# Kernel optimization log

Hardware: AMD Instinct MI355X
Metric: run time of the kernel (lower is better)

## Reference

```python
import jax, jax.numpy as jnp
import numpy as np

B, T, E, H, V = 64, 21, 512, 512, 10000


def _lstm_step(x, h, c, W_ih, W_hh, b):
    # PyTorch LSTMCell gate order: i, f, g, o
    gates = x @ W_ih.T + h @ W_hh.T + b  # [B, 4H]
    i, f, g, o = jnp.split(gates, 4, axis=-1)
    i, f, o = jax.nn.sigmoid(i), jax.nn.sigmoid(f), jax.nn.sigmoid(o)
    g = jnp.tanh(g)
    c_new = f * c + i * g
    h_new = o * jnp.tanh(c_new)
    return h_new, c_new


def setup_inputs() -> dict:
    key = jax.random.key(0)
    ks = jax.random.split(key, 8)
    s_ih = 1.0 / np.sqrt(H)
    return {
        "features": jax.random.normal(ks[0], (B, E), jnp.float32),
        "caption_embedding": jax.random.normal(ks[1], (B, T, E), jnp.float32),
        "W_ih": jax.random.uniform(ks[2], (4 * H, E), jnp.float32, -s_ih, s_ih),
        "W_hh": jax.random.uniform(ks[3], (4 * H, H), jnp.float32, -s_ih, s_ih),
        "b_ih": jax.random.uniform(ks[4], (4 * H,), jnp.float32, -s_ih, s_ih),
        "b_hh": jax.random.uniform(ks[5], (4 * H,), jnp.float32, -s_ih, s_ih),
        "W_lin": jax.random.uniform(ks[6], (V, H), jnp.float32, -s_ih, s_ih),
        "b_lin": jax.random.uniform(ks[7], (V,), jnp.float32, -s_ih, s_ih),
    }


def reference(features, caption_embedding, W_ih, W_hh, b_ih, b_hh, W_lin, b_lin):
    b = b_ih + b_hh
    batch = features.shape[0]
    hidden = W_hh.shape[1]
    h0 = jnp.zeros((batch, hidden), features.dtype)
    c0 = jnp.zeros((batch, hidden), features.dtype)
    # t = 0: consume image features, no output emitted
    h, c = _lstm_step(features, h0, c0, W_ih, W_hh, b)
    # t = 1..T-1: consume caption_embedding[:, t-1], emit linear(h)
    emb_seq = jnp.swapaxes(caption_embedding[:, :-1, :], 0, 1)  # [T-1, B, E]

    def body(carry, x_t):
        h, c = carry
        h, c = _lstm_step(x_t, h, c, W_ih, W_hh, b)
        out = h @ W_lin.T + b_lin  # [B, V]
        return (h, c), out

    _, outs = jax.lax.scan(body, (h, c), emb_seq)  # [T-1, B, V]
    return jnp.swapaxes(outs, 0, 1)  # [B, T-1, V]
```

## Files before the change

kernel.cpp:

```cpp
#include <hip/hip_runtime.h>
#include <hip/hip_bf16.h>


#define NB 64
#define NT 21
#define NE 512
#define NH 512
#define NV 10000
#define G4 2048
#define FLGD 16

typedef __attribute__((ext_vector_type(8))) short bf16x8;
typedef __attribute__((ext_vector_type(4))) float f32x4;
typedef __attribute__((ext_vector_type(4))) unsigned short u16x4;

#define OFF_WIH_HI   0UL
#define OFF_WIH_LO   2097152UL
#define OFF_WHH_HI   4194304UL
#define OFF_WHH_LO   6291456UL
#define OFF_WLIN_HI  8388608UL
#define OFF_XSEQ_HI  18743296UL
#define OFF_XSEQ_LO  20185088UL
#define OFF_BIAS     21626880UL
#define OFF_XIH      21635072UL
#define OFF_GHH      32645120UL
#define OFF_GHL      32776192UL
#define OFF_C        32907264UL
#define OFF_HBUF     33038336UL
#define OFF_FLG      34349056UL

__device__ inline unsigned short f2bf(float f) {
    unsigned int u = __float_as_uint(f);
    unsigned int r = u + 0x7FFFu + ((u >> 16) & 1u);
    return (unsigned short)(r >> 16);
}
__device__ inline float bf2f(unsigned short s) {
    return __uint_as_float(((unsigned int)s) << 16);
}

__device__ __forceinline__ void gl_lds16(const unsigned short* g, unsigned short* l) {
    auto gp = (const __attribute__((address_space(1))) unsigned int*)(unsigned long long)(const void*)g;
    auto lp = (__attribute__((address_space(3))) unsigned int*)(unsigned int)(unsigned long long)(void*)l;
    __builtin_amdgcn_global_load_lds(gp, lp, 16, 0, 0);
}

__device__ __forceinline__ void gl_lds16_sc(const unsigned short* g, unsigned short* l) {
    auto gp = (const __attribute__((address_space(1))) unsigned int*)(unsigned long long)(const void*)g;
    auto lp = (__attribute__((address_space(3))) unsigned int*)(unsigned int)(unsigned long long)(void*)l;
    __builtin_amdgcn_global_load_lds(gp, lp, 16, 0, 17);
}

__device__ __forceinline__ void st4_sc(unsigned int* p, unsigned int v) {
    asm volatile("global_store_dword %0, %1, off sc0 sc1" :: "v"(p), "v"(v) : "memory");
}

__global__ __launch_bounds__(256) void prep_kernel(
    const float* __restrict__ features, const float* __restrict__ cap,
    const float* __restrict__ W_ih, const float* __restrict__ b_ih,
    const float* __restrict__ b_hh, const float* __restrict__ W_lin,
    unsigned char* __restrict__ ws)
{
    const int idx = blockIdx.x * 256 + threadIdx.x;
    unsigned short* wih_hi = (unsigned short*)(ws + OFF_WIH_HI);
    unsigned short* wih_lo = (unsigned short*)(ws + OFF_WIH_LO);
    unsigned short* wlin_hi = (unsigned short*)(ws + OFF_WLIN_HI);
    unsigned short* xs_hi = (unsigned short*)(ws + OFF_XSEQ_HI);
    unsigned short* xs_lo = (unsigned short*)(ws + OFF_XSEQ_LO);
    float* bias = (float*)(ws + OFF_BIAS);

    if (idx < 262144) {
        const int i4 = idx * 4;
        float4 w = *(const float4*)(W_ih + i4);
        u16x4 hi, lo;
        hi.x = f2bf(w.x); lo.x = f2bf(w.x - bf2f(hi.x));
        hi.y = f2bf(w.y); lo.y = f2bf(w.y - bf2f(hi.y));
        hi.z = f2bf(w.z); lo.z = f2bf(w.z - bf2f(hi.z));
        hi.w = f2bf(w.w); lo.w = f2bf(w.w - bf2f(hi.w));
        *(u16x4*)(wih_hi + i4) = hi;
        *(u16x4*)(wih_lo + i4) = lo;
    } else if (idx < 1542144) {
        const int i4 = (idx - 262144) * 4;
        float4 w = *(const float4*)(W_lin + i4);
        u16x4 hi;
        hi.x = f2bf(w.x); hi.y = f2bf(w.y); hi.z = f2bf(w.z); hi.w = f2bf(w.w);
        *(u16x4*)(wlin_hi + i4) = hi;
    } else if (idx < 1714176) {
        const int i4 = (idx - 1542144) * 4;
        const int e = i4 & 511;
        const int b = (i4 >> 9) & 63;
        const int t = i4 >> 15;
        float4 x = (t == 0) ? *(const float4*)(features + b * NE + e)
                            : *(const float4*)(cap + b * (NT * NE) + (t - 1) * NE + e);
        u16x4 hi, lo;
        hi.x = f2bf(x.x); lo.x = f2bf(x.x - bf2f(hi.x));
        hi.y = f2bf(x.y); lo.y = f2bf(x.y - bf2f(hi.y));
        hi.z = f2bf(x.z); lo.z = f2bf(x.z - bf2f(hi.z));
        hi.w = f2bf(x.w); lo.w = f2bf(x.w - bf2f(hi.w));
        *(u16x4*)(xs_hi + i4) = hi;
        *(u16x4*)(xs_lo + i4) = lo;
    } else if (idx < 1714688) {
        const int j = (idx - 1714176) * 4;
        float4 a = *(const float4*)(b_ih + j);
        float4 b = *(const float4*)(b_hh + j);
        *(float4*)(bias + j) = make_float4(a.x + b.x, a.y + b.y, a.z + b.z, a.w + b.w);
    }
}

__global__ __launch_bounds__(512) void fused_persistent(
    unsigned char* __restrict__ ws, const float* __restrict__ W_hh_f,
    const float* __restrict__ b_lin, float* __restrict__ out)
{
    __shared__ unsigned short Hhi[64 * 512];
    __shared__ unsigned short Hlo[64 * 512];
    __shared__ float glf[4096];
    const int tid = threadIdx.x;
    const int lane = tid & 63, wv = tid >> 6;
    const int mf = lane & 15, kg = lane >> 4;

    unsigned int* __restrict__ flg = (unsigned int*)(ws + OFF_C);
    unsigned int* __restrict__ slabctr = (unsigned int*)(ws + OFF_FLG);
    unsigned short* __restrict__ hbuf = (unsigned short*)(ws + OFF_HBUF);
    const unsigned short* __restrict__ wlin = (const unsigned short*)(ws + OFF_WLIN_HI);
    const float* __restrict__ bias = (const float*)(ws + OFF_BIAS);
    float* __restrict__ xih_base = (float*)(ws + OFF_XIH);

    if (blockIdx.x < 32) {
        const int bc = blockIdx.x;
        const int q = wv & 3;
        const int mh = wv >> 2;

        unsigned short* __restrict__ ghh = (unsigned short*)(ws + OFF_GHH);
        unsigned short* __restrict__ ghl = (unsigned short*)(ws + OFF_GHL);

        bf16x8 bh[16], blo[16];
#pragma unroll
        for (int j = 0; j < 16; ++j) {
            const float* src = W_hh_f + (size_t)(q * 512 + bc * 16 + mf) * 512 + j * 32 + kg * 8;
            float4 w0 = *(const float4*)src;
            float4 w1 = *(const float4*)(src + 4);
            float ff[8] = {w0.x, w0.y, w0.z, w0.w, w1.x, w1.y, w1.z, w1.w};
#pragma unroll
            for (int e = 0; e < 8; ++e) {
                const unsigned short h = f2bf(ff[e]);
                bh[j][e] = (short)h;
                blo[j][e] = (short)f2bf(ff[e] - bf2f(h));
            }
        }

        const int crow = tid >> 3;
        const int cp = tid & 7;
        const int c0 = bc * 16 + cp * 2;
        const int jc0 = c0 >> 3;
        float creg0 = 0.f, creg1 = 0.f;

        float2 xp[4];
        auto load_xp = [&](int tt) {
            const float* __restrict__ xq = xih_base + (size_t)tt * NB * G4;
#pragma unroll
            for (int g2 = 0; g2 < 4; ++g2)
                xp[g2] = *(const float2*)&xq[crow * G4 + g2 * 512 + c0];
        };

        if (tid == 0) {
            while (__hip_atomic_load(&slabctr[0], __ATOMIC_RELAXED, __HIP_MEMORY_SCOPE_AGENT) < 16u)
                __builtin_amdgcn_s_sleep(1);
        }
        __syncthreads();
        load_xp(0);

        for (int t = 0; t < NT; ++t) {
            f32x4 acc[2];
            acc[0] = (f32x4){0.f, 0.f, 0.f, 0.f};
            acc[1] = (f32x4){0.f, 0.f, 0.f, 0.f};

            if (t > 0) {
                const int rd = (t + 1) & 1;
                const unsigned short* __restrict__ ghh_r = ghh + rd * (NB * NH);
                const unsigned short* __restrict__ ghl_r = ghl + rd * (NB * NH);
#pragma unroll
                for (int i = 0; i < 8; ++i) {
                    const int s = i * 512 + tid;
                    gl_lds16_sc(ghh_r + s * 8, &Hhi[s * 8]);
                }
#pragma unroll
                for (int i = 0; i < 8; ++i) {
                    const int s = i * 512 + tid;
                    gl_lds16_sc(ghl_r + s * 8, &Hlo[s * 8]);
                }
                asm volatile("s_waitcnt vmcnt(8)" ::: "memory");
                __builtin_amdgcn_s_barrier();
#pragma unroll
                for (int kt = 0; kt < 16; ++kt) {
                    const int j = kt * 4 + kg;
#pragma unroll
                    for (int m = 0; m < 2; ++m) {
                        const int row = mh * 32 + m * 16 + mf;
                        bf16x8 a_hi = *(const bf16x8*)&Hhi[(row * 64 + (j ^ (row & 7))) * 8];
                        acc[m] = __builtin_amdgcn_mfma_f32_16x16x32_bf16(a_hi, bh[kt], acc[m], 0, 0, 0);
                        acc[m] = __builtin_amdgcn_mfma_f32_16x16x32_bf16(a_hi, blo[kt], acc[m], 0, 0, 0);
                    }
                }
                asm volatile("s_waitcnt vmcnt(0)" ::: "memory");
                __builtin_amdgcn_s_barrier();
#pragma unroll
                for (int kt = 0; kt < 16; ++kt) {
                    const int j = kt * 4 + kg;
#pragma unroll
                    for (int m = 0; m < 2; ++m) {
                        const int row = mh * 32 + m * 16 + mf;
                        bf16x8 a_lo = *(const bf16x8*)&Hlo[(row * 64 + (j ^ (row & 7))) * 8];
                        acc[m] = __builtin_amdgcn_mfma_f32_16x16x32_bf16(a_lo, bh[kt], acc[m], 0, 0, 0);
                    }
                }
            }

#pragma unroll
            for (int m = 0; m < 2; ++m) {
                const int row = mh * 32 + m * 16 + kg * 4;
#pragma unroll
                for (int r = 0; r < 4; ++r)
                    glf[(q * 64 + row + r) * 16 + mf] = acc[m][r];
            }
            __syncthreads();

            {
                unsigned short* __restrict__ ghh_w = ghh + (t & 1) * (NB * NH);
                unsigned short* __restrict__ ghl_w = ghl + (t & 1) * (NB * NH);
                const float2 g0 = *(const float2*)&glf[(0 * 64 + crow) * 16 + cp * 2];
                const float2 g1 = *(const float2*)&glf[(1 * 64 + crow) * 16 + cp * 2];
                const float2 g2 = *(const float2*)&glf[(2 * 64 + crow) * 16 + cp * 2];
                const float2 g3 = *(const float2*)&glf[(3 * 64 + crow) * 16 + cp * 2];
                const float gi0 = g0.x + xp[0].x, gi1 = g0.y + xp[0].y;
                const float gf0 = g1.x + xp[1].x, gf1 = g1.y + xp[1].y;
                const float gg0 = g2.x + xp[2].x, gg1 = g2.y + xp[2].y;
                const float go0 = g3.x + xp[3].x, go1 = g3.y + xp[3].y;
                const float i0 = 1.f / (1.f + __expf(-gi0)), i1 = 1.f / (1.f + __expf(-gi1));
                const float f0 = 1.f / (1.f + __expf(-gf0)), f1 = 1.f / (1.f + __expf(-gf1));
                const float ga0 = tanhf(gg0),                ga1 = tanhf(gg1);
                const float o0 = 1.f / (1.f + __expf(-go0)), o1 = 1.f / (1.f + __expf(-go1));
                const float cn0 = f0 * creg0 + i0 * ga0;
                const float cn1 = f1 * creg1 + i1 * ga1;
                creg0 = cn0; creg1 = cn1;
                const float h0 = o0 * tanhf(cn0);
                const float h1 = o1 * tanhf(cn1);
                const unsigned short hi0 = f2bf(h0), hi1 = f2bf(h1);
                const unsigned short lo0 = f2bf(h0 - bf2f(hi0)), lo1 = f2bf(h1 - bf2f(hi1));
                const unsigned int hpack = (unsigned int)hi0 | ((unsigned int)hi1 << 16);
                const unsigned int lpack = (unsigned int)lo0 | ((unsigned int)lo1 << 16);
                const int sw = crow * 512 + ((jc0 ^ (crow & 7)) << 3) + (cp & 3) * 2;
                st4_sc((unsigned int*)&ghh_w[sw], hpack);
                st4_sc((unsigned int*)&ghl_w[sw], lpack);
                if (t >= 1)
                    st4_sc((unsigned int*)&hbuf[(size_t)(t - 1) * (NB * NH) + crow * NH + c0], hpack);
            }

            asm volatile("s_waitcnt vmcnt(0)" ::: "memory");
            __syncthreads();
            if (tid == 0) {
                unsigned int one = 1u;
                unsigned int* fp = flg + ((size_t)t * 32 + bc) * FLGD;
                asm volatile("global_store_dword %0, %1, off sc0 sc1" :: "v"(fp), "v"(one) : "memory");
            }
            if (t < NT - 1) {
                if (tid == 0) {
                    while (__hip_atomic_load(&slabctr[(t + 1) * FLGD], __ATOMIC_RELAXED, __HIP_MEMORY_SCOPE_AGENT) < 16u)
                        __builtin_amdgcn_s_sleep(1);
                }
                __syncthreads();
                load_xp(t + 1);
                if (wv == 0) {
                    const unsigned int* fp = flg + ((size_t)t * 32 + (lane & 31)) * FLGD;
                    while (__hip_atomic_load(fp, __ATOMIC_RELAXED, __HIP_MEMORY_SCOPE_AGENT) == 0u)
                        __builtin_amdgcn_s_sleep(1);
                }
                __syncthreads();
            }
        }
        asm volatile("s_waitcnt vmcnt(0)" ::: "memory");
        return;
    }

    const int g = blockIdx.x - 32;
    const int mw2 = (wv >> 2) * 32, nw2 = (wv & 3) * 32;

    {
        const unsigned short* __restrict__ xh = (const unsigned short*)(ws + OFF_XSEQ_HI);
        const unsigned short* __restrict__ xl = (const unsigned short*)(ws + OFF_XSEQ_LO);
        const unsigned short* __restrict__ wih_h = (const unsigned short*)(ws + OFF_WIH_HI);
        const unsigned short* __restrict__ wih_l = (const unsigned short*)(ws + OFF_WIH_LO);

        unsigned short* Ah2 = Hhi;
        unsigned short* Al2 = Hhi + 4096;
        unsigned short* Bh2 = Hhi + 8192;
        unsigned short* Bl2 = Hhi + 16384;

        const int ntile = (g < 112) ? 2 : 1;
        for (int p = 0; p < ntile; ++p) {
            const int T = (p == 0) ? g : 224 + g;
            const int slab = T >> 4, ct = T & 15;
            const unsigned short* __restrict__ xhA = xh + (size_t)slab * 64 * 512;
            const unsigned short* __restrict__ xlA = xl + (size_t)slab * 64 * 512;

            auto stageA = [&](int buf, int k0) {
                if (tid < 256) {
                    const int s = tid, r = s >> 2, kc = (s & 3) * 8;
                    gl_lds16(xhA + (size_t)r * 512 + k0 + kc, &Ah2[buf * 2048 + s * 8]);
                    gl_lds16(xlA + (size_t)r * 512 + k0 + kc, &Al2[buf * 2048 + s * 8]);
                } else {
#pragma unroll
                    for (int h2 = 0; h2 < 2; ++h2) {
                        const int s = h2 * 256 + (tid - 256), r = s >> 2, kc = (s & 3) * 8;
                        gl_lds16(wih_h + (size_t)(ct * 128 + r) * 512 + k0 + kc, &Bh2[buf * 4096 + s * 8]);
                        gl_lds16(wih_l + (size_t)(ct * 128 + r) * 512 + k0 + kc, &Bl2[buf * 4096 + s * 8]);
                    }
                }
            };

            f32x4 acc2[2][2];
#pragma unroll
            for (int i = 0; i < 2; i++)
#pragma unroll
                for (int j = 0; j < 2; j++) acc2[i][j] = (f32x4){0.f, 0.f, 0.f, 0.f};

            stageA(0, 0);
            for (int kt = 0; kt < 16; ++kt) {
                __syncthreads();
                const int cur = kt & 1;
                if (kt < 15) stageA(cur ^ 1, (kt + 1) * 32);
                bf16x8 ah_[2], al_[2], bh_[2], bl_[2];
#pragma unroll
                for (int i = 0; i < 2; i++) {
                    ah_[i] = *(const bf16x8*)&Ah2[cur * 2048 + (mw2 + i * 16 + mf) * 32 + kg * 8];
                    al_[i] = *(const bf16x8*)&Al2[cur * 2048 + (mw2 + i * 16 + mf) * 32 + kg * 8];
                    bh_[i] = *(const bf16x8*)&Bh2[cur * 4096 + (nw2 + i * 16 + mf) * 32 + kg * 8];
                    bl_[i] = *(const bf16x8*)&Bl2[cur * 4096 + (nw2 + i * 16 + mf) * 32 + kg * 8];
                }
#pragma unroll
                for (int i = 0; i < 2; i++)
#pragma unroll
                    for (int j = 0; j < 2; j++) {
                        acc2[i][j] = __builtin_amdgcn_mfma_f32_16x16x32_bf16(ah_[i], bh_[j], acc2[i][j], 0, 0, 0);
                        acc2[i][j] = __builtin_amdgcn_mfma_f32_16x16x32_bf16(ah_[i], bl_[j], acc2[i][j], 0, 0, 0);
                        acc2[i][j] = __builtin_amdgcn_mfma_f32_16x16x32_bf16(al_[i], bh_[j], acc2[i][j], 0, 0, 0);
                    }
            }
#pragma unroll
            for (int i = 0; i < 2; i++)
#pragma unroll
                for (int j = 0; j < 2; j++) {
                    const int col = ct * 128 + nw2 + j * 16 + mf;
                    const float bb = bias[col];
#pragma unroll
                    for (int r = 0; r < 4; r++) {
                        const int row = slab * 64 + mw2 + i * 16 + kg * 4 + r;
                        st4_sc((unsigned int*)&xih_base[(size_t)row * G4 + col],
                               __float_as_uint(acc2[i][j][r] + bb));
                    }
                }
            asm volatile("s_waitcnt vmcnt(0)" ::: "memory");
            __syncthreads();
            if (tid == 0)
                __hip_atomic_fetch_add(&slabctr[slab * FLGD], 1u, __ATOMIC_RELAXED, __HIP_MEMORY_SCOPE_AGENT);
            __syncthreads();
        }
    }

    const int jt = g % 79;
    const int rshare = g / 79;
    const int nshare = (jt < 66) ? 3 : 2;
    const int n0g = jt * 128;

    unsigned short* __restrict__ AsB = Hhi;
    unsigned short* __restrict__ BsB = Hhi + 4096;

    for (int tt = rshare; tt < NT - 1; tt += nshare) {
        if (wv == 0) {
            const unsigned int* fp = flg + ((size_t)(tt + 1) * 32 + (lane & 31)) * FLGD;
            while (__hip_atomic_load(fp, __ATOMIC_RELAXED, __HIP_MEMORY_SCOPE_AGENT) == 0u)
                __builtin_amdgcn_s_sleep(2);
        }
        __syncthreads();

        const unsigned short* __restrict__ hbA = hbuf + (size_t)tt * (NB * NH);
        auto stageC = [&](int buf, int k0) {
            if (tid < 256) {
                const int s = tid;
                const int r = s >> 2, kcol = (s & 3) * 8;
                gl_lds16_sc(hbA + (size_t)r * 512 + k0 + kcol, &AsB[buf * 2048 + s * 8]);
            } else {
#pragma unroll
                for (int h2 = 0; h2 < 2; ++h2) {
                    const int s = h2 * 256 + (tid - 256);
                    const int r = s >> 2, kcol = (s & 3) * 8;
                    gl_lds16(wlin + (size_t)(n0g + r) * 512 + k0 + kcol, &BsB[buf * 4096 + s * 8]);
                }
            }
        };

        f32x4 acc2[2][2];
#pragma unroll
        for (int i = 0; i < 2; i++)
#pragma unroll
            for (int j = 0; j < 2; j++) acc2[i][j] = (f32x4){0.f, 0.f, 0.f, 0.f};

        stageC(0, 0);
        for (int kt = 0; kt < 16; ++kt) {
            __syncthreads();
            const int cur = kt & 1;
            if (kt < 15) stageC(cur ^ 1, (kt + 1) * 32);
            bf16x8 af[2], bfv[2];
#pragma unroll
            for (int i = 0; i < 2; i++) {
                af[i]  = *(const bf16x8*)&AsB[cur * 2048 + (mw2 + i * 16 + mf) * 32 + kg * 8];
                bfv[i] = *(const bf16x8*)&BsB[cur * 4096 + (nw2 + i * 16 + mf) * 32 + kg * 8];
            }
#pragma unroll
            for (int i = 0; i < 2; i++)
#pragma unroll
                for (int j = 0; j < 2; j++)
                    acc2[i][j] = __builtin_amdgcn_mfma_f32_16x16x32_bf16(af[i], bfv[j], acc2[i][j], 0, 0, 0);
        }
#pragma unroll
        for (int i = 0; i < 2; i++)
#pragma unroll
            for (int j = 0; j < 2; j++) {
                const int col = n0g + nw2 + j * 16 + mf;
                if (col < NV) {
                    const float bl = b_lin[col];
#pragma unroll
                    for (int r = 0; r < 4; r++) {
                        const int b_ = mw2 + i * 16 + kg * 4 + r;
                        out[(size_t)b_ * ((NT - 1) * NV) + (size_t)tt * NV + col] = acc2[i][j][r] + bl;
                    }
                }
            }
        __syncthreads();
    }
}

extern "C" void kernel_launch(void* const* d_in, const int* in_sizes, int n_in,
                              void* d_out, int out_size, void* d_ws, size_t ws_size,
                              hipStream_t stream)
{
    const float* features = (const float*)d_in[0];
    const float* cap      = (const float*)d_in[1];
    const float* W_ih     = (const float*)d_in[2];
    const float* W_hh     = (const float*)d_in[3];
    const float* b_ih     = (const float*)d_in[4];
    const float* b_hh     = (const float*)d_in[5];
    const float* W_lin    = (const float*)d_in[6];
    const float* b_lin    = (const float*)d_in[7];
    float* out = (float*)d_out;
    unsigned char* ws = (unsigned char*)d_ws;

    hipMemsetAsync(ws + OFF_C, 0, (size_t)NT * 32 * FLGD * sizeof(unsigned int), stream);
    hipMemsetAsync(ws + OFF_FLG, 0, (size_t)NT * FLGD * sizeof(unsigned int), stream);

    hipLaunchKernelGGL(prep_kernel, dim3(6698), dim3(256), 0, stream,
                       features, cap, W_ih, b_ih, b_hh, W_lin, ws);
    hipLaunchKernelGGL(fused_persistent, dim3(256), dim3(512), 0, stream, ws, W_hh, b_lin, out);
}
```

Baseline: 251.0 us.

## Fuse prep conversion into persistent kernel and defer W_lin conversion behind recurrence

Removes the separate prep kernel launch and moves the fp32-to-bf16 split of W_ih, inputs and bias into the start of the persistent kernel, guarded by a grid-wide counter. The W_lin bf16 conversion is now done by the 224 non-recurrent blocks after their input-projection GEMM, so it overlaps with the LSTM recurrence, followed by a barrier among those blocks. The recurrent blocks also merge their two waits (slab counter and step flags) into a single wait. The risk is extra spin barriers on all blocks being co-resident, and the start of the recurrence is now delayed until every block finishes prep.

```diff
diff --git a/kernel.cpp b/kernel.cpp
--- a/kernel.cpp
+++ b/kernel.cpp
@@ -53,62 +53,19 @@
 __device__ __forceinline__ void st4_sc(unsigned int* p, unsigned int v) {
     asm volatile("global_store_dword %0, %1, off sc0 sc1" :: "v"(p), "v"(v) : "memory");
 }
-
-__global__ __launch_bounds__(256) void prep_kernel(
+__device__ __forceinline__ void st8_sc(unsigned short* p, u16x4 v) {
+    asm volatile("global_store_dwordx2 %0, %1, off sc0 sc1" :: "v"(p), "v"(v) : "memory");
+}
+__device__ __forceinline__ void st16_sc(float* p, f32x4 v) {
+    asm volatile("global_store_dwordx4 %0, %1, off sc0 sc1" :: "v"(p), "v"(v) : "memory");
+}
+
+__global__ __launch_bounds__(512) void fused_all(
     const float* __restrict__ features, const float* __restrict__ cap,
-    const float* __restrict__ W_ih, const float* __restrict__ b_ih,
-    const float* __restrict__ b_hh, const float* __restrict__ W_lin,
-    unsigned char* __restrict__ ws)
-{
-    const int idx = blockIdx.x * 256 + threadIdx.x;
-    unsigned short* wih_hi = (unsigned short*)(ws + OFF_WIH_HI);
-    unsigned short* wih_lo = (unsigned short*)(ws + OFF_WIH_LO);
-    unsigned short* wlin_hi = (unsigned short*)(ws + OFF_WLIN_HI);
-    unsigned short* xs_hi = (unsigned short*)(ws + OFF_XSEQ_HI);
-    unsigned short* xs_lo = (unsigned short*)(ws + OFF_XSEQ_LO);
-    float* bias = (float*)(ws + OFF_BIAS);
-
-    if (idx < 262144) {
-        const int i4 = idx * 4;
-        float4 w = *(const float4*)(W_ih + i4);
-        u16x4 hi, lo;
-        hi.x = f2bf(w.x); lo.x = f2bf(w.x - bf2f(hi.x));
-        hi.y = f2bf(w.y); lo.y = f2bf(w.y - bf2f(hi.y));
-        hi.z = f2bf(w.z); lo.z = f2bf(w.z - bf2f(hi.z));
-        hi.w = f2bf(w.w); lo.w = f2bf(w.w - bf2f(hi.w));
-        *(u16x4*)(wih_hi + i4) = hi;
-        *(u16x4*)(wih_lo + i4) = lo;
-    } else if (idx < 1542144) {
-        const int i4 = (idx - 262144) * 4;
-        float4 w = *(const float4*)(W_lin + i4);
-        u16x4 hi;
-        hi.x = f2bf(w.x); hi.y = f2bf(w.y); hi.z = f2bf(w.z); hi.w = f2bf(w.w);
-        *(u16x4*)(wlin_hi + i4) = hi;
-    } else if (idx < 1714176) {
-        const int i4 = (idx - 1542144) * 4;
-        const int e = i4 & 511;
-        const int b = (i4 >> 9) & 63;
-        const int t = i4 >> 15;
-        float4 x = (t == 0) ? *(const float4*)(features + b * NE + e)
-                            : *(const float4*)(cap + b * (NT * NE) + (t - 1) * NE + e);
-        u16x4 hi, lo;
-        hi.x = f2bf(x.x); lo.x = f2bf(x.x - bf2f(hi.x));
-        hi.y = f2bf(x.y); lo.y = f2bf(x.y - bf2f(hi.y));
-        hi.z = f2bf(x.z); lo.z = f2bf(x.z - bf2f(hi.z));
-        hi.w = f2bf(x.w); lo.w = f2bf(x.w - bf2f(hi.w));
-        *(u16x4*)(xs_hi + i4) = hi;
-        *(u16x4*)(xs_lo + i4) = lo;
-    } else if (idx < 1714688) {
-        const int j = (idx - 1714176) * 4;
-        float4 a = *(const float4*)(b_ih + j);
-        float4 b = *(const float4*)(b_hh + j);
-        *(float4*)(bias + j) = make_float4(a.x + b.x, a.y + b.y, a.z + b.z, a.w + b.w);
-    }
-}
-
-__global__ __launch_bounds__(512) void fused_persistent(
-    unsigned char* __restrict__ ws, const float* __restrict__ W_hh_f,
-    const float* __restrict__ b_lin, float* __restrict__ out)
+    const float* __restrict__ W_ih_f, const float* __restrict__ W_hh_f,
+    const float* __restrict__ b_ih, const float* __restrict__ b_hh,
+    const float* __restrict__ W_lin_f, const float* __restrict__ b_lin,
+    float* __restrict__ out, unsigned char* __restrict__ ws)
 {
     __shared__ unsigned short Hhi[64 * 512];
     __shared__ unsigned short Hlo[64 * 512];
@@ -120,9 +77,55 @@
     unsigned int* __restrict__ flg = (unsigned int*)(ws + OFF_C);
     unsigned int* __restrict__ slabctr = (unsigned int*)(ws + OFF_FLG);
     unsigned short* __restrict__ hbuf = (unsigned short*)(ws + OFF_HBUF);
-    const unsigned short* __restrict__ wlin = (const unsigned short*)(ws + OFF_WLIN_HI);
     const float* __restrict__ bias = (const float*)(ws + OFF_BIAS);
     float* __restrict__ xih_base = (float*)(ws + OFF_XIH);
+
+    {
+        unsigned short* wih_hi = (unsigned short*)(ws + OFF_WIH_HI);
+        unsigned short* wih_lo = (unsigned short*)(ws + OFF_WIH_LO);
+        unsigned short* xs_hi = (unsigned short*)(ws + OFF_XSEQ_HI);
+        unsigned short* xs_lo = (unsigned short*)(ws + OFF_XSEQ_LO);
+        float* bias_w = (float*)(ws + OFF_BIAS);
+        int idx = blockIdx.x * 512 + tid;
+        for (int it = 0; it < 4; ++it, idx += 131072) {
+            if (idx < 262144) {
+                const int i4 = idx * 4;
+                float4 w = *(const float4*)(W_ih_f + i4);
+                u16x4 hi, lo;
+                hi.x = f2bf(w.x); lo.x = f2bf(w.x - bf2f(hi.x));
+                hi.y = f2bf(w.y); lo.y = f2bf(w.y - bf2f(hi.y));
+                hi.z = f2bf(w.z); lo.z = f2bf(w.z - bf2f(hi.z));
+                hi.w = f2bf(w.w); lo.w = f2bf(w.w - bf2f(hi.w));
+                st8_sc(wih_hi + i4, hi);
+                st8_sc(wih_lo + i4, lo);
+            } else if (idx < 434176) {
+                const int i4 = (idx - 262144) * 4;
+                const int e = i4 & 511;
+                const int b = (i4 >> 9) & 63;
+                const int t2 = i4 >> 15;
+                float4 x = (t2 == 0) ? *(const float4*)(features + b * NE + e)
+                                     : *(const float4*)(cap + b * (NT * NE) + (t2 - 1) * NE + e);
+                u16x4 hi, lo;
+                hi.x = f2bf(x.x); lo.x = f2bf(x.x - bf2f(hi.x));
+                hi.y = f2bf(x.y); lo.y = f2bf(x.y - bf2f(hi.y));
+                hi.z = f2bf(x.z); lo.z = f2bf(x.z - bf2f(hi.z));
+                hi.w = f2bf(x.w); lo.w = f2bf(x.w - bf2f(hi.w));
+                st8_sc(xs_hi + i4, hi);
+                st8_sc(xs_lo + i4, lo);
+            } else if (idx < 434688) {
+                const int j = (idx - 434176) * 4;
+                float4 a = *(const float4*)(b_ih + j);
+                float4 b = *(const float4*)(b_hh + j);
+                f32x4 s;
+                s[0] = a.x + b.x; s[1] = a.y + b.y; s[2] = a.z + b.z; s[3] = a.w + b.w;
+                st16_sc(bias_w + j, s);
+            }
+        }
+        asm volatile("s_waitcnt vmcnt(0)" ::: "memory");
+        __syncthreads();
+        if (tid == 0)
+            __hip_atomic_fetch_add(&slabctr[24 * FLGD], 1u, __ATOMIC_RELAXED, __HIP_MEMORY_SCOPE_AGENT);
+    }
 
     if (blockIdx.x < 32) {
         const int bc = blockIdx.x;
@@ -262,18 +265,19 @@
                 asm volatile("global_store_dword %0, %1, off sc0 sc1" :: "v"(fp), "v"(one) : "memory");
             }
             if (t < NT - 1) {
-                if (tid == 0) {
-                    while (__hip_atomic_load(&slabctr[(t + 1) * FLGD], __ATOMIC_RELAXED, __HIP_MEMORY_SCOPE_AGENT) < 16u)
-                        __builtin_amdgcn_s_sleep(1);
+                if (wv == 0) {
+                    if (lane < 32) {
+                        const unsigned int* fp = flg + ((size_t)t * 32 + lane) * FLGD;
+                        while (__hip_atomic_load(fp, __ATOMIC_RELAXED, __HIP_MEMORY_SCOPE_AGENT) == 0u)
+                            __builtin_amdgcn_s_sleep(1);
+                    } else if (lane == 32) {
+                        const unsigned int* sp = slabctr + (size_t)(t + 1) * FLGD;
+                        while (__hip_atomic_load(sp, __ATOMIC_RELAXED, __HIP_MEMORY_SCOPE_AGENT) < 16u)
+                            __builtin_amdgcn_s_sleep(1);
+                    }
                 }
                 __syncthreads();
                 load_xp(t + 1);
-                if (wv == 0) {
-                    const unsigned int* fp = flg + ((size_t)t * 32 + (lane & 31)) * FLGD;
-                    while (__hip_atomic_load(fp, __ATOMIC_RELAXED, __HIP_MEMORY_SCOPE_AGENT) == 0u)
-                        __builtin_amdgcn_s_sleep(1);
-                }
-                __syncthreads();
             }
         }
         asm volatile("s_waitcnt vmcnt(0)" ::: "memory");
@@ -282,6 +286,12 @@
 
     const int g = blockIdx.x - 32;
     const int mw2 = (wv >> 2) * 32, nw2 = (wv & 3) * 32;
+
+    if (tid == 0) {
+        while (__hip_atomic_load(&slabctr[24 * FLGD], __ATOMIC_RELAXED, __HIP_MEMORY_SCOPE_AGENT) < 256u)
+            __builtin_amdgcn_s_sleep(1);
+    }
+    __syncthreads();
 
     {
         const unsigned short* __restrict__ xh = (const unsigned short*)(ws + OFF_XSEQ_HI);
@@ -365,6 +375,29 @@
         }
     }
 
+    {
+        unsigned short* wlin_w = (unsigned short*)(ws + OFF_WLIN_HI);
+        int idx = g * 512 + tid;
+        for (int it = 0; it < 12; ++it, idx += 114688) {
+            if (idx < 1280000) {
+                const int i4 = idx * 4;
+                float4 w = *(const float4*)(W_lin_f + i4);
+                u16x4 hi;
+                hi.x = f2bf(w.x); hi.y = f2bf(w.y); hi.z = f2bf(w.z); hi.w = f2bf(w.w);
+                st8_sc(wlin_w + i4, hi);
+            }
+        }
+        asm volatile("s_waitcnt vmcnt(0)" ::: "memory");
+        __syncthreads();
+        if (tid == 0) {
+            __hip_atomic_fetch_add(&slabctr[25 * FLGD], 1u, __ATOMIC_RELAXED, __HIP_MEMORY_SCOPE_AGENT);
+            while (__hip_atomic_load(&slabctr[25 * FLGD], __ATOMIC_RELAXED, __HIP_MEMORY_SCOPE_AGENT) < 224u)
+                __builtin_amdgcn_s_sleep(1);
+        }
+        __syncthreads();
+    }
+
+    const unsigned short* __restrict__ wlin = (const unsigned short*)(ws + OFF_WLIN_HI);
     const int jt = g % 79;
     const int rshare = g / 79;
     const int nshare = (jt < 66) ? 3 : 2;
@@ -453,10 +486,9 @@
     float* out = (float*)d_out;
     unsigned char* ws = (unsigned char*)d_ws;
 
-    hipMemsetAsync(ws + OFF_C, 0, (size_t)NT * 32 * FLGD * sizeof(unsigned int), stream);
-    hipMemsetAsync(ws + OFF_FLG, 0, (size_t)NT * FLGD * sizeof(unsigned int), stream);
-
-    hipLaunchKernelGGL(prep_kernel, dim3(6698), dim3(256), 0, stream,
-                       features, cap, W_ih, b_ih, b_hh, W_lin, ws);
-    hipLaunchKernelGGL(fused_persistent, dim3(256), dim3(512), 0, stream, ws, W_hh, b_lin, out);
-}
+    (void)hipMemsetAsync(ws + OFF_C, 0, (size_t)NT * 32 * FLGD * sizeof(unsigned int), stream);
+    (void)hipMemsetAsync(ws + OFF_FLG, 0, (size_t)32 * FLGD * sizeof(unsigned int), stream);
+
+    hipLaunchKernelGGL(fused_all, dim3(256), dim3(512), 0, stream,
+                       features, cap, W_ih, W_hh, b_ih, b_hh, W_lin, b_lin, out, ws);
+}
```

New measurement: 269.1 us. 7.2% more time.
